# Performance work log

Measured on AMD Instinct MI355X. Metric: run time of the kernel, lower is better.

Reference implementation:

```python
import jax, jax.numpy as jnp
import numpy as np

B, L, D = 512, 33, 4096
P, K, H = 64, 512, 128  # proj_dim, topk, head hidden
LN_EPS = 1e-5


def setup_inputs() -> dict:
    key = jax.random.key(0)
    ks = jax.random.split(key, 12)
    s = lambda fan_in: 1.0 / np.sqrt(fan_in)
    return {
        "x": jax.random.normal(ks[0], (B, L, D), dtype=jnp.float32),
        "Wp": jax.random.uniform(ks[1], (P, L), jnp.float32, -s(L), s(L)),
        "bp": jax.random.uniform(ks[2], (P,), jnp.float32, -s(L), s(L)),
        "ws": jax.random.uniform(ks[3], (P,), jnp.float32, -s(P), s(P)),
        "bs": jax.random.uniform(ks[4], (), jnp.float32, -s(P), s(P)),
        "gamma": jnp.ones((P,), jnp.float32),
        "beta": jnp.zeros((P,), jnp.float32),
        "W1": jax.random.uniform(ks[5], (H, P), jnp.float32, -s(P), s(P)),
        "b1": jax.random.uniform(ks[6], (H,), jnp.float32, -s(P), s(P)),
        "W2": jax.random.uniform(ks[7], (2, H), jnp.float32, -s(H), s(H)),
        "b2": jax.random.uniform(ks[8], (2,), jnp.float32, -s(H), s(H)),
    }


def reference(x, Wp, bp, ws, bs, gamma, beta, W1, b1, W2, b2):
    # x: (B, L, D) -> per-dim layer trajectories projected to P
    h = jnp.einsum("bld,pl->bdp", x, Wp) + bp           # (B, D, P)
    scores = jnp.einsum("bdp,p->bd", h, ws) + bs         # (B, D)
    topk_scores, topk_idx = jax.lax.top_k(scores, K)     # (B, K)
    w = jax.nn.softmax(topk_scores, axis=-1)             # (B, K)
    topk_h = jnp.take_along_axis(h, topk_idx[:, :, None], axis=1)  # (B, K, P)
    out = jnp.einsum("bkp,bk->bp", topk_h, w)            # (B, P)
    # head: LayerNorm -> Linear -> GELU -> Linear (dropout in eval = identity)
    mu = jnp.mean(out, axis=-1, keepdims=True)
    var = jnp.mean((out - mu) ** 2, axis=-1, keepdims=True)
    z = (out - mu) * jax.lax.rsqrt(var + LN_EPS) * gamma + beta
    z = jax.nn.gelu(z @ W1.T + b1, approximate=False)
    return z @ W2.T + b2                                  # (B, 2)
```

## Files before the change

kernel.cpp:

```cpp
#include <hip/hip_runtime.h>
#include <math.h>

#define NB 512
#define LL 33
#define DD 4096
#define PP 64
#define KK 512
#define HH 128
#define LN_EPS 1e-5f
#define NT 256

__device__ __forceinline__ unsigned fkey(float s) {
    unsigned u = __float_as_uint(s);
    return (u & 0x80000000u) ? ~u : (u | 0x80000000u);
}

__device__ __forceinline__ float waveMax(float v) {
    #pragma unroll
    for (int o = 32; o > 0; o >>= 1) v = fmaxf(v, __shfl_xor(v, o));
    return v;
}
__device__ __forceinline__ float waveSum(float v) {
    #pragma unroll
    for (int o = 32; o > 0; o >>= 1) v += __shfl_xor(v, o);
    return v;
}

__global__ __launch_bounds__(NT) void sda_kernel(
    const float* __restrict__ x,
    const float* __restrict__ Wp, const float* __restrict__ bp,
    const float* __restrict__ ws, const float* __restrict__ bsp,
    const float* __restrict__ gamma, const float* __restrict__ beta,
    const float* __restrict__ W1, const float* __restrict__ b1,
    const float* __restrict__ W2, const float* __restrict__ b2,
    float* __restrict__ out)
{
    __shared__ __align__(16) float s_w[DD];
    __shared__ __align__(16) float s_xc[LL * 256];
    __shared__ float s_v[LL];
    __shared__ unsigned s_hist[4][256];
    __shared__ unsigned s_scanA[256];
    __shared__ unsigned s_scanB[256];
    __shared__ float s_red[4];
    __shared__ float s_y[LL];
    __shared__ float s_o[PP];
    __shared__ float s_g[HH];
    __shared__ float s_c, s_m, s_S;
    __shared__ unsigned s_prefix, s_kk, s_ceq;

    const int t = threadIdx.x;
    const int lane = t & 63;
    const int wv = t >> 6;
    const int b = blockIdx.x;
    const float* __restrict__ xb = x + (size_t)b * (LL * DD);

    if (t < LL) {
        float a = 0.f;
        for (int p = 0; p < PP; ++p) a += Wp[p * LL + t] * ws[p];
        s_v[t] = a;
    } else if (t == LL) {
        float a = bsp[0];
        for (int p = 0; p < PP; ++p) a += ws[p] * bp[p];
        s_c = a;
    }
    if (t == 0) { s_prefix = 0u; s_kk = KK; s_ceq = 0u; }
    __syncthreads();

    const float c0 = s_c;
    float4* s_w4 = (float4*)s_w;
    float4* s_xc4 = (float4*)s_xc;
    float4 acc[4];
    #pragma unroll
    for (int i = 0; i < 4; ++i) acc[i] = make_float4(c0, c0, c0, c0);
    for (int l = 0; l < LL; ++l) {
        const float vl = s_v[l];
        const float4* row = (const float4*)(xb + l * DD);
        const float4 xv0 = row[t];
        const float4 xv1 = row[t + NT];
        const float4 xv2 = row[t + 2 * NT];
        const float4 xv3 = row[t + 3 * NT];
        if (t < 64) s_xc4[l * 64 + t] = xv0;
        acc[0].x += vl * xv0.x; acc[0].y += vl * xv0.y; acc[0].z += vl * xv0.z; acc[0].w += vl * xv0.w;
        acc[1].x += vl * xv1.x; acc[1].y += vl * xv1.y; acc[1].z += vl * xv1.z; acc[1].w += vl * xv1.w;
        acc[2].x += vl * xv2.x; acc[2].y += vl * xv2.y; acc[2].z += vl * xv2.z; acc[2].w += vl * xv2.w;
        acc[3].x += vl * xv3.x; acc[3].y += vl * xv3.y; acc[3].z += vl * xv3.z; acc[3].w += vl * xv3.w;
    }
    unsigned ukey[16];
    float lmax = -INFINITY;
    #pragma unroll
    for (int i = 0; i < 4; ++i) {
        s_w4[t + i * NT] = acc[i];
        ukey[4 * i + 0] = fkey(acc[i].x);
        ukey[4 * i + 1] = fkey(acc[i].y);
        ukey[4 * i + 2] = fkey(acc[i].z);
        ukey[4 * i + 3] = fkey(acc[i].w);
        lmax = fmaxf(fmaxf(lmax, fmaxf(acc[i].x, acc[i].y)), fmaxf(acc[i].z, acc[i].w));
    }
    lmax = waveMax(lmax);
    if (lane == 0) s_red[wv] = lmax;
    __syncthreads();
    if (t == 0) s_m = fmaxf(fmaxf(s_red[0], s_red[1]), fmaxf(s_red[2], s_red[3]));
    __syncthreads();

    for (int shift = 24; shift >= 0; shift -= 8) {
        for (int i = t; i < 4 * 256; i += NT) ((unsigned*)s_hist)[i] = 0u;
        __syncthreads();
        const unsigned pfx = s_prefix;
        const unsigned hm = (shift == 24) ? 0u : (0xFFFFFFFFu << (shift + 8));
        #pragma unroll
        for (int i = 0; i < 16; ++i) {
            const unsigned u = ukey[i];
            if ((u & hm) == pfx)
                atomicAdd(&s_hist[wv][(u >> shift) & 255u], 1u);
        }
        __syncthreads();
        s_scanA[t] = s_hist[0][t] + s_hist[1][t] + s_hist[2][t] + s_hist[3][t];
        __syncthreads();
        unsigned* src = s_scanA;
        unsigned* dst = s_scanB;
        for (int off = 1; off < 256; off <<= 1) {
            dst[t] = src[t] + ((t + off < 256) ? src[t + off] : 0u);
            __syncthreads();
            unsigned* tmp = src; src = dst; dst = tmp;
        }
        const unsigned kk = s_kk;
        const unsigned mine = src[t];
        const unsigned above = (t == 255) ? 0u : src[t + 1];
        __syncthreads();
        if (mine >= kk && above < kk) {
            s_prefix = pfx | ((unsigned)t << shift);
            s_kk = kk - above;
            s_ceq = mine - above;
        }
        __syncthreads();
    }
    const unsigned T = s_prefix;
    const unsigned need_eq = s_kk;
    const unsigned count_eq = s_ceq;
    const float m = s_m;

    if (count_eq == need_eq) {
        float lsum = 0.f;
        #pragma unroll
        for (int i = 0; i < 4; ++i) {
            float4 w;
            w.x = (ukey[4 * i + 0] >= T) ? expf(acc[i].x - m) : 0.f;
            w.y = (ukey[4 * i + 1] >= T) ? expf(acc[i].y - m) : 0.f;
            w.z = (ukey[4 * i + 2] >= T) ? expf(acc[i].z - m) : 0.f;
            w.w = (ukey[4 * i + 3] >= T) ? expf(acc[i].w - m) : 0.f;
            s_w4[t + i * NT] = w;
            lsum += w.x + w.y + w.z + w.w;
        }
        lsum = waveSum(lsum);
        if (lane == 0) s_red[wv] = lsum;
        __syncthreads();
        if (t == 0) s_S = s_red[0] + s_red[1] + s_red[2] + s_red[3];
        __syncthreads();
    } else {
        __syncthreads();
        if (t == 0) {
            unsigned taken = 0;
            float S = 0.f;
            for (int d = 0; d < DD; ++d) {
                const float s = s_w[d];
                const unsigned u = fkey(s);
                float w = 0.f;
                if (u > T) w = expf(s - m);
                else if (u == T && taken < need_eq) { w = expf(s - m); ++taken; }
                s_w[d] = w;
                S += w;
            }
            s_S = S;
        }
        __syncthreads();
    }
    const float invS = 1.0f / s_S;

    for (int l = wv; l < LL; l += 4) {
        const float4* row = (const float4*)(xb + l * DD);
        float a = 0.f;
        {
            const float4 xv = s_xc4[l * 64 + lane];
            const float4 w4 = s_w4[lane];
            a += w4.x * xv.x + w4.y * xv.y + w4.z * xv.z + w4.w * xv.w;
        }
        #pragma unroll
        for (int j = 1; j < 16; ++j) {
            const int f = lane + j * 64;
            const float4 xv = row[f];
            const float4 w4 = s_w4[f];
            a += w4.x * xv.x + w4.y * xv.y + w4.z * xv.z + w4.w * xv.w;
        }
        a = waveSum(a);
        if (lane == 0) s_y[l] = a;
    }
    __syncthreads();

    if (t < PP) {
        float a = 0.f;
        for (int l = 0; l < LL; ++l) a += Wp[t * LL + l] * s_y[l];
        s_o[t] = a * invS + bp[t];
    }
    __syncthreads();
    if (wv == 0) {
        const float o = s_o[lane];
        const float mu = waveSum(o) * (1.f / PP);
        const float dv = o - mu;
        const float var = waveSum(dv * dv) * (1.f / PP);
        s_o[lane] = dv * rsqrtf(var + LN_EPS) * gamma[lane] + beta[lane];
    }
    __syncthreads();
    if (t < HH) {
        float a = b1[t];
        for (int p = 0; p < PP; ++p) a += W1[t * PP + p] * s_o[p];
        s_g[t] = 0.5f * a * (1.f + erff(a * 0.70710678118654752440f));
    }
    __syncthreads();
    if (t < 2) {
        float a = b2[t];
        for (int j = 0; j < HH; ++j) a += W2[t * HH + j] * s_g[j];
        out[b * 2 + t] = a;
    }
}

extern "C" void kernel_launch(void* const* d_in, const int* in_sizes, int n_in,
                              void* d_out, int out_size, void* d_ws, size_t ws_size,
                              hipStream_t stream) {
    const float* x     = (const float*)d_in[0];
    const float* Wp    = (const float*)d_in[1];
    const float* bp    = (const float*)d_in[2];
    const float* ws    = (const float*)d_in[3];
    const float* bs    = (const float*)d_in[4];
    const float* gamma = (const float*)d_in[5];
    const float* beta  = (const float*)d_in[6];
    const float* W1    = (const float*)d_in[7];
    const float* b1    = (const float*)d_in[8];
    const float* W2    = (const float*)d_in[9];
    const float* b2    = (const float*)d_in[10];
    float* out = (float*)d_out;
    hipLaunchKernelGGL(sda_kernel, dim3(NB), dim3(NT), 0, stream,
                       x, Wp, bp, ws, bs, gamma, beta, W1, b1, W2, b2, out);
}
```

Before: 438.3 us.

## Double block size, software-pipeline score loads, reverse second-pass row order

Raises the block to 512 threads so each thread holds two float4 columns instead of four, and prefetches the next layer row while accumulating the current one. This is meant to raise memory-level parallelism and latency hiding in the dominant streaming pass. The weighted-sum pass now walks rows and columns in reverse order, so the data most recently brought in by the first pass is revisited first while it may still sit in cache. The histogram and scan are gated to the first 256 threads, and the block keeps the same large shared-memory footprint, which may limit occupancy.

```diff
diff --git a/kernel.cpp b/kernel.cpp
--- a/kernel.cpp
+++ b/kernel.cpp
@@ -8,7 +8,8 @@
 #define KK 512
 #define HH 128
 #define LN_EPS 1e-5f
-#define NT 256
+#define NT 512
+#define NW (NT / 64)
 
 __device__ __forceinline__ unsigned fkey(float s) {
     unsigned u = __float_as_uint(s);
@@ -38,10 +39,10 @@
     __shared__ __align__(16) float s_w[DD];
     __shared__ __align__(16) float s_xc[LL * 256];
     __shared__ float s_v[LL];
-    __shared__ unsigned s_hist[4][256];
+    __shared__ unsigned s_hist[NW][256];
     __shared__ unsigned s_scanA[256];
     __shared__ unsigned s_scanB[256];
-    __shared__ float s_red[4];
+    __shared__ float s_red[NW];
     __shared__ float s_y[LL];
     __shared__ float s_o[PP];
     __shared__ float s_g[HH];
@@ -69,68 +70,79 @@
     const float c0 = s_c;
     float4* s_w4 = (float4*)s_w;
     float4* s_xc4 = (float4*)s_xc;
-    float4 acc[4];
-    #pragma unroll
-    for (int i = 0; i < 4; ++i) acc[i] = make_float4(c0, c0, c0, c0);
-    for (int l = 0; l < LL; ++l) {
+    const float4* rp = (const float4*)xb;
+    float4 cur0 = rp[t];
+    float4 cur1 = rp[t + NT];
+    float4 acc0 = make_float4(c0, c0, c0, c0);
+    float4 acc1 = acc0;
+    for (int l = 0; l < LL - 1; ++l) {
+        const float4* np = rp + 1024;
+        const float4 nxt0 = np[t];
+        const float4 nxt1 = np[t + NT];
         const float vl = s_v[l];
-        const float4* row = (const float4*)(xb + l * DD);
-        const float4 xv0 = row[t];
-        const float4 xv1 = row[t + NT];
-        const float4 xv2 = row[t + 2 * NT];
-        const float4 xv3 = row[t + 3 * NT];
-        if (t < 64) s_xc4[l * 64 + t] = xv0;
-        acc[0].x += vl * xv0.x; acc[0].y += vl * xv0.y; acc[0].z += vl * xv0.z; acc[0].w += vl * xv0.w;
-        acc[1].x += vl * xv1.x; acc[1].y += vl * xv1.y; acc[1].z += vl * xv1.z; acc[1].w += vl * xv1.w;
-        acc[2].x += vl * xv2.x; acc[2].y += vl * xv2.y; acc[2].z += vl * xv2.z; acc[2].w += vl * xv2.w;
-        acc[3].x += vl * xv3.x; acc[3].y += vl * xv3.y; acc[3].z += vl * xv3.z; acc[3].w += vl * xv3.w;
-    }
-    unsigned ukey[16];
-    float lmax = -INFINITY;
-    #pragma unroll
-    for (int i = 0; i < 4; ++i) {
-        s_w4[t + i * NT] = acc[i];
-        ukey[4 * i + 0] = fkey(acc[i].x);
-        ukey[4 * i + 1] = fkey(acc[i].y);
-        ukey[4 * i + 2] = fkey(acc[i].z);
-        ukey[4 * i + 3] = fkey(acc[i].w);
-        lmax = fmaxf(fmaxf(lmax, fmaxf(acc[i].x, acc[i].y)), fmaxf(acc[i].z, acc[i].w));
-    }
+        if (t < 64) s_xc4[l * 64 + t] = cur0;
+        acc0.x += vl * cur0.x; acc0.y += vl * cur0.y; acc0.z += vl * cur0.z; acc0.w += vl * cur0.w;
+        acc1.x += vl * cur1.x; acc1.y += vl * cur1.y; acc1.z += vl * cur1.z; acc1.w += vl * cur1.w;
+        cur0 = nxt0; cur1 = nxt1; rp = np;
+    }
+    {
+        const float vl = s_v[LL - 1];
+        if (t < 64) s_xc4[(LL - 1) * 64 + t] = cur0;
+        acc0.x += vl * cur0.x; acc0.y += vl * cur0.y; acc0.z += vl * cur0.z; acc0.w += vl * cur0.w;
+        acc1.x += vl * cur1.x; acc1.y += vl * cur1.y; acc1.z += vl * cur1.z; acc1.w += vl * cur1.w;
+    }
+
+    unsigned ukey[8];
+    s_w4[t] = acc0;
+    s_w4[t + NT] = acc1;
+    ukey[0] = fkey(acc0.x); ukey[1] = fkey(acc0.y); ukey[2] = fkey(acc0.z); ukey[3] = fkey(acc0.w);
+    ukey[4] = fkey(acc1.x); ukey[5] = fkey(acc1.y); ukey[6] = fkey(acc1.z); ukey[7] = fkey(acc1.w);
+    float lmax = fmaxf(fmaxf(fmaxf(acc0.x, acc0.y), fmaxf(acc0.z, acc0.w)),
+                       fmaxf(fmaxf(acc1.x, acc1.y), fmaxf(acc1.z, acc1.w)));
     lmax = waveMax(lmax);
     if (lane == 0) s_red[wv] = lmax;
     __syncthreads();
-    if (t == 0) s_m = fmaxf(fmaxf(s_red[0], s_red[1]), fmaxf(s_red[2], s_red[3]));
+    if (t == 0) {
+        float m = s_red[0];
+        for (int i = 1; i < NW; ++i) m = fmaxf(m, s_red[i]);
+        s_m = m;
+    }
     __syncthreads();
 
     for (int shift = 24; shift >= 0; shift -= 8) {
-        for (int i = t; i < 4 * 256; i += NT) ((unsigned*)s_hist)[i] = 0u;
+        for (int i = t; i < NW * 256; i += NT) ((unsigned*)s_hist)[i] = 0u;
         __syncthreads();
         const unsigned pfx = s_prefix;
         const unsigned hm = (shift == 24) ? 0u : (0xFFFFFFFFu << (shift + 8));
         #pragma unroll
-        for (int i = 0; i < 16; ++i) {
+        for (int i = 0; i < 8; ++i) {
             const unsigned u = ukey[i];
             if ((u & hm) == pfx)
                 atomicAdd(&s_hist[wv][(u >> shift) & 255u], 1u);
         }
         __syncthreads();
-        s_scanA[t] = s_hist[0][t] + s_hist[1][t] + s_hist[2][t] + s_hist[3][t];
+        if (t < 256) {
+            unsigned a = 0;
+            for (int w = 0; w < NW; ++w) a += s_hist[w][t];
+            s_scanA[t] = a;
+        }
         __syncthreads();
         unsigned* src = s_scanA;
         unsigned* dst = s_scanB;
         for (int off = 1; off < 256; off <<= 1) {
-            dst[t] = src[t] + ((t + off < 256) ? src[t + off] : 0u);
+            if (t < 256) dst[t] = src[t] + ((t + off < 256) ? src[t + off] : 0u);
             __syncthreads();
             unsigned* tmp = src; src = dst; dst = tmp;
         }
-        const unsigned kk = s_kk;
-        const unsigned mine = src[t];
-        const unsigned above = (t == 255) ? 0u : src[t + 1];
-        __syncthreads();
-        if (mine >= kk && above < kk) {
-            s_prefix = pfx | ((unsigned)t << shift);
-            s_kk = kk - above;
-            s_ceq = mine - above;
+        if (t < 256) {
+            const unsigned kk = s_kk;
+            const unsigned mine = src[t];
+            const unsigned above = (t == 255) ? 0u : src[t + 1];
+            if (mine >= kk && above < kk) {
+                s_prefix = pfx | ((unsigned)t << shift);
+                s_kk = kk - above;
+                s_ceq = mine - above;
+            }
         }
         __syncthreads();
     }
@@ -140,21 +152,26 @@
     const float m = s_m;
 
     if (count_eq == need_eq) {
-        float lsum = 0.f;
-        #pragma unroll
-        for (int i = 0; i < 4; ++i) {
-            float4 w;
-            w.x = (ukey[4 * i + 0] >= T) ? expf(acc[i].x - m) : 0.f;
-            w.y = (ukey[4 * i + 1] >= T) ? expf(acc[i].y - m) : 0.f;
-            w.z = (ukey[4 * i + 2] >= T) ? expf(acc[i].z - m) : 0.f;
-            w.w = (ukey[4 * i + 3] >= T) ? expf(acc[i].w - m) : 0.f;
-            s_w4[t + i * NT] = w;
-            lsum += w.x + w.y + w.z + w.w;
-        }
+        float4 w0, w1;
+        w0.x = (ukey[0] >= T) ? expf(acc0.x - m) : 0.f;
+        w0.y = (ukey[1] >= T) ? expf(acc0.y - m) : 0.f;
+        w0.z = (ukey[2] >= T) ? expf(acc0.z - m) : 0.f;
+        w0.w = (ukey[3] >= T) ? expf(acc0.w - m) : 0.f;
+        w1.x = (ukey[4] >= T) ? expf(acc1.x - m) : 0.f;
+        w1.y = (ukey[5] >= T) ? expf(acc1.y - m) : 0.f;
+        w1.z = (ukey[6] >= T) ? expf(acc1.z - m) : 0.f;
+        w1.w = (ukey[7] >= T) ? expf(acc1.w - m) : 0.f;
+        s_w4[t] = w0;
+        s_w4[t + NT] = w1;
+        float lsum = w0.x + w0.y + w0.z + w0.w + w1.x + w1.y + w1.z + w1.w;
         lsum = waveSum(lsum);
         if (lane == 0) s_red[wv] = lsum;
         __syncthreads();
-        if (t == 0) s_S = s_red[0] + s_red[1] + s_red[2] + s_red[3];
+        if (t == 0) {
+            float S = 0.f;
+            for (int i = 0; i < NW; ++i) S += s_red[i];
+            s_S = S;
+        }
         __syncthreads();
     } else {
         __syncthreads();
@@ -176,23 +193,26 @@
     }
     const float invS = 1.0f / s_S;
 
-    for (int l = wv; l < LL; l += 4) {
-        const float4* row = (const float4*)(xb + l * DD);
-        float a = 0.f;
-        {
-            const float4 xv = s_xc4[l * 64 + lane];
-            const float4 w4 = s_w4[lane];
-            a += w4.x * xv.x + w4.y * xv.y + w4.z * xv.z + w4.w * xv.w;
-        }
-        #pragma unroll
-        for (int j = 1; j < 16; ++j) {
-            const int f = lane + j * 64;
-            const float4 xv = row[f];
-            const float4 w4 = s_w4[f];
-            a += w4.x * xv.x + w4.y * xv.y + w4.z * xv.z + w4.w * xv.w;
-        }
-        a = waveSum(a);
-        if (lane == 0) s_y[l] = a;
+    for (int k = 4; k >= 0; --k) {
+        const int l = wv + NW * k;
+        if (l < LL) {
+            const float4* row = (const float4*)(xb + l * DD);
+            float a = 0.f;
+            #pragma unroll
+            for (int j = 15; j >= 1; --j) {
+                const int f = lane + j * 64;
+                const float4 xv = row[f];
+                const float4 w4 = s_w4[f];
+                a += w4.x * xv.x + w4.y * xv.y + w4.z * xv.z + w4.w * xv.w;
+            }
+            {
+                const float4 xv = s_xc4[l * 64 + lane];
+                const float4 w4 = s_w4[lane];
+                a += w4.x * xv.x + w4.y * xv.y + w4.z * xv.z + w4.w * xv.w;
+            }
+            a = waveSum(a);
+            if (lane == 0) s_y[l] = a;
+        }
     }
     __syncthreads();
 
```

Measured after the change: 462.8 us. 1.06x slower.
